# Kernel tuning notes

Measured on AMD Instinct MI355X. Metric: run time of the kernel, lower is better.

## Reference

```python
import jax, jax.numpy as jnp
import numpy as np

# Production-scale graph dims (see shape_source)
N = 50000      # nodes
E = 800000     # edges (avg degree 16)
C_IN = 128     # input feature dim
H = 96         # hidden (per species: prey X and predator Y)
C_OUT = 40     # num_classes
L = 5          # LVConv layers
DT = 0.05      # integration step


def setup_inputs() -> dict:
    key = jax.random.key(0)
    ks = jax.random.split(key, 14)
    x = jax.random.normal(ks[0], (N, C_IN), jnp.float32)
    edge_index = jax.random.randint(ks[1], (2, E), 0, N, dtype=jnp.int32)
    # lift linears
    Wx = jax.random.normal(ks[2], (C_IN, H), jnp.float32) / np.sqrt(C_IN)
    bx = jnp.zeros((H,), jnp.float32)
    Wy = jax.random.normal(ks[3], (C_IN, H), jnp.float32) / np.sqrt(C_IN)
    by = jnp.zeros((H,), jnp.float32)
    # per-layer Lotka-Volterra coefficients (per-channel), small positive scale
    alpha = 0.1 * jax.random.uniform(ks[4], (L, H), jnp.float32)
    beta  = 0.1 * jax.random.uniform(ks[5], (L, H), jnp.float32)
    gamma = 0.1 * jax.random.uniform(ks[6], (L, H), jnp.float32)
    delta = 0.1 * jax.random.uniform(ks[7], (L, H), jnp.float32)
    # readout on concat([X, Y])
    Wr = jax.random.normal(ks[8], (2 * H, C_OUT), jnp.float32) / np.sqrt(2 * H)
    br = jnp.zeros((C_OUT,), jnp.float32)
    return {"x": x, "edge_index": edge_index, "Wx": Wx, "bx": bx,
            "Wy": Wy, "by": by, "alpha": alpha, "beta": beta,
            "gamma": gamma, "delta": delta, "Wr": Wr, "br": br}


def reference(x, edge_index, Wx, bx, Wy, by, alpha, beta, gamma, delta, Wr, br):
    src, dst = edge_index[0], edge_index[1]
    # in-degree for mean aggregation over incoming edges
    deg = jax.ops.segment_sum(jnp.ones((E,), x.dtype), dst, num_segments=N)
    deg_inv = (1.0 / jnp.maximum(deg, 1.0))[:, None]  # [N,1]

    def mean_agg(v):  # [N,H] -> [N,H] neighbor mean (src -> dst)
        return jax.ops.segment_sum(v[src], dst, num_segments=N) * deg_inv

    # lift to prey (X) and predator (Y) populations
    X = jnp.tanh(x @ Wx + bx)
    Y = jnp.tanh(x @ Wy + by)
    # dropout is identity in eval mode (training=False)
    for l in range(L):
        aggX = mean_agg(X)
        aggY = mean_agg(Y)
        # explicit-Euler Lotka-Volterra dynamics on the graph
        Xn = X + DT * X * (alpha[l] - beta[l] * aggY)
        Yn = Y + DT * Y * (-gamma[l] + delta[l] * aggX)
        X, Y = Xn, Yn
    h = jnp.concatenate([X, Y], axis=-1)  # [N, 2H]
    return h @ Wr + br
```

## Files before the change

### kernel.cpp

```cpp
#include <hip/hip_runtime.h>
#include <hip/hip_bf16.h>
#include <hip/hip_fp16.h>


#define HDIM 96
#define CIN 128
#define COUT 40
#define NLAYER 5
#define DTC 0.05f

#define BK_SHIFT 7
#define BK_SIZE 128
#define EPB 4096

typedef float  vfloat2 __attribute__((ext_vector_type(2)));
typedef float  vfloat4 __attribute__((ext_vector_type(4)));
typedef short  vshort8 __attribute__((ext_vector_type(8)));

__device__ __forceinline__ unsigned bf16_rne(float f) {
    unsigned u = __float_as_uint(f);
    return (u + 0x7fffu + ((u >> 16) & 1u)) >> 16;
}

__device__ __forceinline__ unsigned pack_bf16_pair(float xf, float yf) {
    return bf16_rne(xf) | (bf16_rne(yf) << 16);
}

__device__ __forceinline__ unsigned pack_f16_pair(float a, float b) {
    unsigned ha = (unsigned)__half_as_ushort(__float2half_rn(a));
    unsigned hb = (unsigned)__half_as_ushort(__float2half_rn(b));
    return ha | (hb << 16);
}

__device__ __forceinline__ float f16_lo(unsigned u) {
    return __half2float(__ushort_as_half((unsigned short)(u & 0xffffu)));
}
__device__ __forceinline__ float f16_hi(unsigned u) {
    return __half2float(__ushort_as_half((unsigned short)(u >> 16)));
}

__device__ __forceinline__ unsigned pack_fp8_quad(float x0, float y0, float x1, float y1) {
    int lo = __builtin_amdgcn_cvt_pk_fp8_f32(x0, y0, 0, false);
    int full = __builtin_amdgcn_cvt_pk_fp8_f32(x1, y1, lo, true);
    return (unsigned)full;
}


__global__ __launch_bounds__(256) void bhist_kernel(const int* __restrict__ dst,
                                                    int* __restrict__ ghist, int E, int NB) {
    __shared__ int h[512];
    for (int i = threadIdx.x; i < NB; i += 256) h[i] = 0;
    __syncthreads();
    int base = blockIdx.x * EPB;
    int end = min(E, base + EPB);
    for (int e = base + threadIdx.x; e < end; e += 256)
        atomicAdd(&h[dst[e] >> BK_SHIFT], 1);
    __syncthreads();
    for (int i = threadIdx.x; i < NB; i += 256)
        if (h[i]) atomicAdd(&ghist[i], h[i]);
}

__global__ void bscan_kernel(const int* __restrict__ ghist, int* __restrict__ bbase,
                             int* __restrict__ bcursor, int* __restrict__ rowptr,
                             int NB, int N, int E) {
    __shared__ int sd[512];
    int t = threadIdx.x;
    int v = (t < NB) ? ghist[t] : 0;
    sd[t] = v;
    __syncthreads();
    for (int off = 1; off < 512; off <<= 1) {
        int tv = (t >= off) ? sd[t - off] : 0;
        __syncthreads();
        sd[t] += tv;
        __syncthreads();
    }
    if (t < NB) {
        int b = sd[t] - v;
        bbase[t] = b;
        bcursor[t] = b;
    }
    if (t == 0) { bbase[NB] = E; rowptr[N] = E; }
}

__global__ __launch_bounds__(256) void bscatter_kernel(
    const int* __restrict__ src, const int* __restrict__ dst,
    int* __restrict__ bcursor, unsigned* __restrict__ packed, int E, int NB) {
    __shared__ int h[512];
    __shared__ int cur[512];
    for (int i = threadIdx.x; i < NB; i += 256) h[i] = 0;
    __syncthreads();
    int base = blockIdx.x * EPB;
    int end = min(E, base + EPB);
    for (int e = base + threadIdx.x; e < end; e += 256)
        atomicAdd(&h[dst[e] >> BK_SHIFT], 1);
    __syncthreads();
    for (int i = threadIdx.x; i < NB; i += 256)
        cur[i] = h[i] ? atomicAdd(&bcursor[i], h[i]) : 0;
    __syncthreads();
    for (int e = base + threadIdx.x; e < end; e += 256) {
        int d = dst[e];
        int b = d >> BK_SHIFT;
        int pos = atomicAdd(&cur[b], 1);
        packed[pos] = (unsigned)src[e] | ((unsigned)(d & (BK_SIZE - 1)) << 17);
    }
}

__global__ __launch_bounds__(256) void bcsr_kernel(
    const unsigned* __restrict__ packed, const int* __restrict__ bbase,
    int* __restrict__ rowptr, float* __restrict__ dinv, int* __restrict__ csr,
    int N, int NB) {
    __shared__ int ldeg[BK_SIZE];
    __shared__ int sscan[BK_SIZE];
    __shared__ int lcur[BK_SIZE];
    int b = blockIdx.x;
    int t = threadIdx.x;
    int lo = bbase[b], hi = bbase[b + 1];
    if (t < BK_SIZE) ldeg[t] = 0;
    __syncthreads();
    for (int e = lo + t; e < hi; e += 256)
        atomicAdd(&ldeg[(packed[e] >> 17) & (BK_SIZE - 1)], 1);
    __syncthreads();
    if (t < BK_SIZE) sscan[t] = ldeg[t];
    __syncthreads();
    for (int off = 1; off < BK_SIZE; off <<= 1) {
        int tv = (t < BK_SIZE && t >= off) ? sscan[t - off] : 0;
        __syncthreads();
        if (t < BK_SIZE) sscan[t] += tv;
        __syncthreads();
    }
    if (t < BK_SIZE) {
        int excl = sscan[t] - ldeg[t];
        int gpos = lo + excl;
        lcur[t] = gpos;
        int node = b * BK_SIZE + t;
        if (node < N) {
            rowptr[node] = gpos;
            dinv[node] = 1.0f / fmaxf((float)ldeg[t], 1.0f);
        }
    }
    __syncthreads();
    for (int e = lo + t; e < hi; e += 256) {
        unsigned p = packed[e];
        int l = (p >> 17) & (BK_SIZE - 1);
        int pos = atomicAdd(&lcur[l], 1);
        csr[pos] = (int)(p & 0x1FFFFu);
    }
}


__global__ __launch_bounds__(256) void wprep_kernel(
    const float* __restrict__ Wx, const float* __restrict__ bx,
    const float* __restrict__ Wy, const float* __restrict__ by,
    unsigned short* __restrict__ WcT, float* __restrict__ bc) {
    int t = blockIdx.x * blockDim.x + threadIdx.x;
    if (t < 192 * 128) {
        int cc = t >> 7;
        int k = t & 127;
        int h = cc >> 1;
        float w = (cc & 1) ? Wy[k * HDIM + h] : Wx[k * HDIM + h];
        WcT[cc * 128 + k] = (unsigned short)bf16_rne(w);
    }
    if (t < 192) {
        int h = t >> 1;
        bc[t] = (t & 1) ? by[h] : bx[h];
    }
}


#define LW_STRIDE 136

__global__ __launch_bounds__(256) void lift_mfma_kernel(
    const float* __restrict__ x, const unsigned short* __restrict__ WcT,
    const float* __restrict__ bc, unsigned* __restrict__ S,
    unsigned* __restrict__ F, int N) {
    __shared__ unsigned short sW[192 * LW_STRIDE];
    __shared__ float sBc[192];
    int t = threadIdx.x;

    {
        const unsigned* g = (const unsigned*)WcT;
        unsigned* s = (unsigned*)sW;
        for (int i = t; i < 192 * 64; i += 256) {
            int cc = i >> 6;
            int kp = i & 63;
            s[cc * (LW_STRIDE / 2) + kp] = g[i];
        }
    }
    if (t < 192) sBc[t] = bc[t];
    __syncthreads();

    int wv = t >> 6;
    int lane = t & 63;
    int quad = lane >> 4;
    int m = lane & 15;
    int mbase = blockIdx.x * 64 + wv * 16;

    int anode = mbase + m;
    if (anode >= N) anode = N - 1;
    const float* xrow = x + (size_t)anode * CIN;

    vfloat4 acc[12];
#pragma unroll
    for (int i = 0; i < 12; i++) acc[i] = (vfloat4){0.f, 0.f, 0.f, 0.f};

#pragma unroll
    for (int kt = 0; kt < 4; kt++) {
        int k0 = kt * 32 + quad * 8;
        float4 xa = *(const float4*)(xrow + k0);
        float4 xb = *(const float4*)(xrow + k0 + 4);
        uint4 ua;
        ua.x = pack_bf16_pair(xa.x, xa.y);
        ua.y = pack_bf16_pair(xa.z, xa.w);
        ua.z = pack_bf16_pair(xb.x, xb.y);
        ua.w = pack_bf16_pair(xb.z, xb.w);
        vshort8 a = *(vshort8*)&ua;
#pragma unroll
        for (int nt = 0; nt < 12; nt++) {
            vshort8 b = *(const vshort8*)&sW[(nt * 16 + m) * LW_STRIDE + k0];
            acc[nt] = __builtin_amdgcn_mfma_f32_16x16x32_bf16(a, b, acc[nt], 0, 0, 0);
        }
    }

#pragma unroll
    for (int nt = 0; nt < 12; nt++) {
        int ccb = nt * 16 + m;
        float bco = sBc[ccb];
#pragma unroll
        for (int r = 0; r < 4; r++) {
            int node = mbase + quad * 4 + r;
            float v = tanhf(acc[nt][r] + bco);
            float v1 = __shfl_xor(v, 1);
            unsigned u = (unsigned)(__builtin_amdgcn_cvt_pk_fp8_f32(v, v1, 0, false) & 0xffff);
            unsigned w = u | (((unsigned)__shfl_xor((int)u, 2)) << 16);
            unsigned hp = pack_f16_pair(v, v1);
            if (node < N) {
                if ((m & 1) == 0) S[(size_t)node * 96 + (ccb >> 1)] = hp;
                if ((m & 3) == 0) F[(size_t)node * 48 + (ccb >> 2)] = w;
            }
        }
    }
}


#define LWPB 4

__global__ __launch_bounds__(256) void layer_kernel(
    const unsigned* __restrict__ F, const unsigned* __restrict__ S,
    unsigned* __restrict__ Sn, unsigned* __restrict__ Fn,
    const int* __restrict__ rowptr, const int* __restrict__ csr,
    const float* __restrict__ deg_inv,
    const float* __restrict__ alpha, const float* __restrict__ beta,
    const float* __restrict__ gamma, const float* __restrict__ delta,
    int N) {
    int wave = threadIdx.x >> 6;
    int lane = threadIdx.x & 63;
    int node = blockIdx.x * LWPB + wave;
    if (node >= N) return;

    int beg = rowptr[node];
    int cnt = rowptr[node + 1] - beg;
    bool act = (lane < 48);

    float ax0 = 0.f, ay0 = 0.f, ax1 = 0.f, ay1 = 0.f;

#define UNPACK_ACC(u)                                                      \
    do {                                                                   \
        vfloat2 p0 = __builtin_amdgcn_cvt_pk_f32_fp8((int)(u), false);     \
        vfloat2 p1 = __builtin_amdgcn_cvt_pk_f32_fp8((int)(u), true);      \
        ax0 += p0.x; ay0 += p0.y; ax1 += p1.x; ay1 += p1.y;                \
    } while (0)

    for (int base = 0; base < cnt; base += 64) {
        int m = min(64, cnt - base);
        int sidx = (lane < m) ? csr[beg + base + lane] : 0;
        int j = 0;
        for (; j + 8 <= m; j += 8) {
            int s0 = __shfl(sidx, j);
            int s1 = __shfl(sidx, j + 1);
            int s2 = __shfl(sidx, j + 2);
            int s3 = __shfl(sidx, j + 3);
            int s4 = __shfl(sidx, j + 4);
            int s5 = __shfl(sidx, j + 5);
            int s6 = __shfl(sidx, j + 6);
            int s7 = __shfl(sidx, j + 7);
            if (act) {
                unsigned u0 = F[(size_t)s0 * 48 + lane];
                unsigned u1 = F[(size_t)s1 * 48 + lane];
                unsigned u2 = F[(size_t)s2 * 48 + lane];
                unsigned u3 = F[(size_t)s3 * 48 + lane];
                unsigned u4 = F[(size_t)s4 * 48 + lane];
                unsigned u5 = F[(size_t)s5 * 48 + lane];
                unsigned u6 = F[(size_t)s6 * 48 + lane];
                unsigned u7 = F[(size_t)s7 * 48 + lane];
                UNPACK_ACC(u0); UNPACK_ACC(u1); UNPACK_ACC(u2); UNPACK_ACC(u3);
                UNPACK_ACC(u4); UNPACK_ACC(u5); UNPACK_ACC(u6); UNPACK_ACC(u7);
            }
        }
        for (; j < m; j++) {
            int s = __shfl(sidx, j);
            if (act) {
                unsigned u = F[(size_t)s * 48 + lane];
                UNPACK_ACC(u);
            }
        }
    }
#undef UNPACK_ACC

    float dinv = deg_inv[node];
    if (act) {
        ax0 *= dinv; ay0 *= dinv; ax1 *= dinv; ay1 *= dinv;
        float2 a2 = ((const float2*)alpha)[lane];
        float2 b2 = ((const float2*)beta)[lane];
        float2 g2 = ((const float2*)gamma)[lane];
        float2 d2 = ((const float2*)delta)[lane];
        uint2 su = ((const uint2*)(S + (size_t)node * 96))[lane];
        float vx = f16_lo(su.x), vy = f16_hi(su.x);
        float vz = f16_lo(su.y), vw = f16_hi(su.y);
        float ox = vx + DTC * vx * (a2.x - b2.x * ay0);
        float oy = vy + DTC * vy * (-g2.x + d2.x * ax0);
        float oz = vz + DTC * vz * (a2.y - b2.y * ay1);
        float ow = vw + DTC * vw * (-g2.y + d2.y * ax1);
        ((uint2*)(Sn + (size_t)node * 96))[lane] =
            make_uint2(pack_f16_pair(ox, oy), pack_f16_pair(oz, ow));
        if (Fn)
            Fn[(size_t)node * 48 + lane] = pack_fp8_quad(ox, oy, oz, ow);
    }
}


#define WG_STRIDE 200

__global__ __launch_bounds__(256) void readout_mfma_kernel(
    const unsigned short* __restrict__ sh, const float* __restrict__ Wr,
    const float* __restrict__ br, float* __restrict__ out, int N) {
    __shared__ unsigned short sW[48 * WG_STRIDE];
    __shared__ float sB[48];
    int t = threadIdx.x;

    for (int i = t; i < 48 * 192; i += 256) {
        int n = i / 192;
        int kk = i - n * 192;
        int h = kk >> 1;
        float w = 0.f;
        if (n < COUT) w = (kk & 1) ? Wr[(HDIM + h) * COUT + n] : Wr[h * COUT + n];
        sW[n * WG_STRIDE + kk] = __half_as_ushort(__float2half_rn(w));
    }
    if (t < 48) sB[t] = (t < COUT) ? br[t] : 0.f;
    __syncthreads();

    int wv = t >> 6;
    int lane = t & 63;
    int quad = lane >> 4;
    int m = lane & 15;
    int mbase = blockIdx.x * 64 + wv * 16;

    int anode = mbase + m;
    if (anode >= N) anode = N - 1;
    const unsigned short* arow = sh + (size_t)anode * 192;

    vfloat4 acc0 = {0.f, 0.f, 0.f, 0.f};
    vfloat4 acc1 = {0.f, 0.f, 0.f, 0.f};
    vfloat4 acc2 = {0.f, 0.f, 0.f, 0.f};

#pragma unroll
    for (int kt = 0; kt < 6; kt++) {
        int k0 = kt * 32 + quad * 8;
        vshort8 a = *(const vshort8*)(arow + k0);
        vshort8 b0 = *(const vshort8*)&sW[(0 * 16 + m) * WG_STRIDE + k0];
        vshort8 b1 = *(const vshort8*)&sW[(1 * 16 + m) * WG_STRIDE + k0];
        vshort8 b2 = *(const vshort8*)&sW[(2 * 16 + m) * WG_STRIDE + k0];
        acc0 = __builtin_amdgcn_mfma_f32_16x16x32_f16(a, b0, acc0, 0, 0, 0);
        acc1 = __builtin_amdgcn_mfma_f32_16x16x32_f16(a, b1, acc1, 0, 0, 0);
        acc2 = __builtin_amdgcn_mfma_f32_16x16x32_f16(a, b2, acc2, 0, 0, 0);
    }

    float bo0 = sB[m];
    float bo1 = sB[16 + m];
    float bo2 = (m < 8) ? sB[32 + m] : 0.f;
#pragma unroll
    for (int r = 0; r < 4; r++) {
        int node = mbase + quad * 4 + r;
        if (node < N) {
            float* orow = out + (size_t)node * COUT;
            orow[m] = acc0[r] + bo0;
            orow[16 + m] = acc1[r] + bo1;
            if (m < 8) orow[32 + m] = acc2[r] + bo2;
        }
    }
}


extern "C" void kernel_launch(void* const* d_in, const int* in_sizes, int n_in,
                              void* d_out, int out_size, void* d_ws, size_t ws_size,
                              hipStream_t stream) {
    const float* x     = (const float*)d_in[0];
    const int*   ei    = (const int*)d_in[1];
    const float* Wx    = (const float*)d_in[2];
    const float* bx    = (const float*)d_in[3];
    const float* Wy    = (const float*)d_in[4];
    const float* by    = (const float*)d_in[5];
    const float* alpha = (const float*)d_in[6];
    const float* beta  = (const float*)d_in[7];
    const float* gamma = (const float*)d_in[8];
    const float* delta = (const float*)d_in[9];
    const float* Wr    = (const float*)d_in[10];
    const float* br    = (const float*)d_in[11];

    const int N = in_sizes[0] / CIN;
    const int E = in_sizes[1] / 2;
    const int NB = (N + BK_SIZE - 1) >> BK_SHIFT;
    const int nchunk = (E + EPB - 1) / EPB;

    char* ws = (char*)d_ws;
    size_t off = 0;
    auto alloc = [&](size_t bytes) -> void* {
        off = (off + 255) & ~(size_t)255;
        void* p = ws + off;
        off += bytes;
        return p;
    };
    int* ghist     = (int*)alloc((size_t)NB * sizeof(int));
    int* bbase     = (int*)alloc((size_t)(NB + 1) * sizeof(int));
    int* bcursor   = (int*)alloc((size_t)NB * sizeof(int));
    unsigned* pckd = (unsigned*)alloc((size_t)E * sizeof(unsigned));
    int* rowptr    = (int*)alloc((size_t)(N + 1) * sizeof(int));
    int* csr       = (int*)alloc((size_t)E * sizeof(int));
    float* dinv    = (float*)alloc((size_t)N * sizeof(float));
    unsigned* Sa   = (unsigned*)alloc((size_t)N * 96 * sizeof(unsigned));
    unsigned* Sb   = (unsigned*)alloc((size_t)N * 96 * sizeof(unsigned));
    unsigned* Fa   = (unsigned*)alloc((size_t)N * 48 * sizeof(unsigned));
    unsigned* Fb   = (unsigned*)alloc((size_t)N * 48 * sizeof(unsigned));
    unsigned short* WcT = (unsigned short*)alloc((size_t)192 * 128 * sizeof(unsigned short));
    float* bc      = (float*)alloc((size_t)192 * sizeof(float));
    (void)ws_size;

    const int* e_src = ei;
    const int* e_dst = ei + E;

    hipMemsetAsync(ghist, 0, (size_t)NB * sizeof(int), stream);

    bhist_kernel<<<nchunk, 256, 0, stream>>>(e_dst, ghist, E, NB);
    bscan_kernel<<<1, 512, 0, stream>>>(ghist, bbase, bcursor, rowptr, NB, N, E);
    bscatter_kernel<<<nchunk, 256, 0, stream>>>(e_src, e_dst, bcursor, pckd, E, NB);
    bcsr_kernel<<<NB, 256, 0, stream>>>(pckd, bbase, rowptr, dinv, csr, N, NB);

    wprep_kernel<<<(192 * 128 + 255) / 256, 256, 0, stream>>>(Wx, bx, Wy, by, WcT, bc);
    lift_mfma_kernel<<<(N + 63) / 64, 256, 0, stream>>>(x, WcT, bc, Sa, Fa, N);

    const unsigned* Sc = Sa;
    unsigned* Snx = Sb;
    const unsigned* Fc = Fa;
    unsigned* Fnx = Fb;
    for (int l = 0; l < NLAYER; l++) {
        bool last = (l == NLAYER - 1);
        layer_kernel<<<(N + LWPB - 1) / LWPB, LWPB * 64, 0, stream>>>(
            Fc, Sc, Snx, last ? (unsigned*)nullptr : Fnx,
            rowptr, csr, dinv,
            alpha + l * HDIM, beta + l * HDIM, gamma + l * HDIM, delta + l * HDIM, N);
        const unsigned* ts = Sc; Sc = Snx; Snx = (unsigned*)ts;
        const unsigned* tf = Fc; Fc = Fnx; Fnx = (unsigned*)tf;
    }

    readout_mfma_kernel<<<(N + 63) / 64, 256, 0, stream>>>(
        (const unsigned short*)Sc, Wr, br, (float*)d_out, N);
}
```

Baseline: 354.7 us.

## Process four nodes per wave with 16-lane groups and 12-byte gathers

The layer kernel now assigns one 16-lane group per node, so each wave handles four nodes instead of one. Each lane fetches three packed fp8 words (uint3) per neighbor row, where before 48 of 64 lanes fetched one word each. This removes idle lanes and cuts per-node wave overhead, and it issues more independent loads per wave. In exchange, each lane holds more accumulator registers, neighbor loops inside a wave diverge when degrees differ, and the 12-byte accesses may be less aligned.

```diff
diff --git a/kernel.cpp b/kernel.cpp
--- a/kernel.cpp
+++ b/kernel.cpp
@@ -242,8 +242,6 @@
 }
 
 
-#define LWPB 4
-
 __global__ __launch_bounds__(256) void layer_kernel(
     const unsigned* __restrict__ F, const unsigned* __restrict__ S,
     unsigned* __restrict__ Sn, unsigned* __restrict__ Fn,
@@ -254,76 +252,85 @@
     int N) {
     int wave = threadIdx.x >> 6;
     int lane = threadIdx.x & 63;
-    int node = blockIdx.x * LWPB + wave;
-    if (node >= N) return;
-
-    int beg = rowptr[node];
-    int cnt = rowptr[node + 1] - beg;
-    bool act = (lane < 48);
-
-    float ax0 = 0.f, ay0 = 0.f, ax1 = 0.f, ay1 = 0.f;
-
-#define UNPACK_ACC(u)                                                      \
-    do {                                                                   \
-        vfloat2 p0 = __builtin_amdgcn_cvt_pk_f32_fp8((int)(u), false);     \
-        vfloat2 p1 = __builtin_amdgcn_cvt_pk_f32_fp8((int)(u), true);      \
-        ax0 += p0.x; ay0 += p0.y; ax1 += p1.x; ay1 += p1.y;                \
+    int li = lane & 15;
+    int gbase = lane & 48;
+
+    int node = (blockIdx.x * 4 + wave) * 4 + (lane >> 4);
+    bool nvalid = node < N;
+    int nclamp = nvalid ? node : N - 1;
+    int beg = rowptr[nclamp];
+    int cnt = nvalid ? (rowptr[nclamp + 1] - beg) : 0;
+
+    float ac[12];
+#pragma unroll
+    for (int i = 0; i < 12; i++) ac[i] = 0.f;
+
+#define UNP(u, k)                                                           \
+    do {                                                                    \
+        vfloat2 p0 = __builtin_amdgcn_cvt_pk_f32_fp8((int)(u), false);      \
+        vfloat2 p1 = __builtin_amdgcn_cvt_pk_f32_fp8((int)(u), true);       \
+        ac[4*(k)+0] += p0.x; ac[4*(k)+1] += p0.y;                           \
+        ac[4*(k)+2] += p1.x; ac[4*(k)+3] += p1.y;                           \
     } while (0)
-
-    for (int base = 0; base < cnt; base += 64) {
-        int m = min(64, cnt - base);
-        int sidx = (lane < m) ? csr[beg + base + lane] : 0;
+#define UNP3(u)  do { UNP((u).x, 0); UNP((u).y, 1); UNP((u).z, 2); } while (0)
+
+    for (int base = 0; base < cnt; base += 16) {
+        int m = min(16, cnt - base);
+        int sidx = (li < m) ? csr[beg + base + li] : 0;
         int j = 0;
-        for (; j + 8 <= m; j += 8) {
-            int s0 = __shfl(sidx, j);
-            int s1 = __shfl(sidx, j + 1);
-            int s2 = __shfl(sidx, j + 2);
-            int s3 = __shfl(sidx, j + 3);
-            int s4 = __shfl(sidx, j + 4);
-            int s5 = __shfl(sidx, j + 5);
-            int s6 = __shfl(sidx, j + 6);
-            int s7 = __shfl(sidx, j + 7);
-            if (act) {
-                unsigned u0 = F[(size_t)s0 * 48 + lane];
-                unsigned u1 = F[(size_t)s1 * 48 + lane];
-                unsigned u2 = F[(size_t)s2 * 48 + lane];
-                unsigned u3 = F[(size_t)s3 * 48 + lane];
-                unsigned u4 = F[(size_t)s4 * 48 + lane];
-                unsigned u5 = F[(size_t)s5 * 48 + lane];
-                unsigned u6 = F[(size_t)s6 * 48 + lane];
-                unsigned u7 = F[(size_t)s7 * 48 + lane];
-                UNPACK_ACC(u0); UNPACK_ACC(u1); UNPACK_ACC(u2); UNPACK_ACC(u3);
-                UNPACK_ACC(u4); UNPACK_ACC(u5); UNPACK_ACC(u6); UNPACK_ACC(u7);
-            }
+        for (; j + 4 <= m; j += 4) {
+            int s0 = __shfl(sidx, gbase + j);
+            int s1 = __shfl(sidx, gbase + j + 1);
+            int s2 = __shfl(sidx, gbase + j + 2);
+            int s3 = __shfl(sidx, gbase + j + 3);
+            uint3 u0 = ((const uint3*)(F + (size_t)s0 * 48))[li];
+            uint3 u1 = ((const uint3*)(F + (size_t)s1 * 48))[li];
+            uint3 u2 = ((const uint3*)(F + (size_t)s2 * 48))[li];
+            uint3 u3 = ((const uint3*)(F + (size_t)s3 * 48))[li];
+            UNP3(u0); UNP3(u1); UNP3(u2); UNP3(u3);
         }
         for (; j < m; j++) {
-            int s = __shfl(sidx, j);
-            if (act) {
-                unsigned u = F[(size_t)s * 48 + lane];
-                UNPACK_ACC(u);
-            }
-        }
-    }
-#undef UNPACK_ACC
-
-    float dinv = deg_inv[node];
-    if (act) {
-        ax0 *= dinv; ay0 *= dinv; ax1 *= dinv; ay1 *= dinv;
-        float2 a2 = ((const float2*)alpha)[lane];
-        float2 b2 = ((const float2*)beta)[lane];
-        float2 g2 = ((const float2*)gamma)[lane];
-        float2 d2 = ((const float2*)delta)[lane];
-        uint2 su = ((const uint2*)(S + (size_t)node * 96))[lane];
+            int s = __shfl(sidx, gbase + j);
+            uint3 u = ((const uint3*)(F + (size_t)s * 48))[li];
+            UNP3(u);
+        }
+    }
+#undef UNP3
+#undef UNP
+
+    if (!nvalid) return;
+
+    float dinv = deg_inv[nclamp];
+    const uint2* srow = (const uint2*)(S + (size_t)node * 96);
+    unsigned so[6];
+    unsigned fo[3];
+#pragma unroll
+    for (int k = 0; k < 3; k++) {
+        int p = 3 * li + k;
+        float2 a2 = ((const float2*)alpha)[p];
+        float2 b2 = ((const float2*)beta)[p];
+        float2 g2 = ((const float2*)gamma)[p];
+        float2 d2 = ((const float2*)delta)[p];
+        uint2 su = srow[p];
         float vx = f16_lo(su.x), vy = f16_hi(su.x);
         float vz = f16_lo(su.y), vw = f16_hi(su.y);
-        float ox = vx + DTC * vx * (a2.x - b2.x * ay0);
-        float oy = vy + DTC * vy * (-g2.x + d2.x * ax0);
-        float oz = vz + DTC * vz * (a2.y - b2.y * ay1);
-        float ow = vw + DTC * vw * (-g2.y + d2.y * ax1);
-        ((uint2*)(Sn + (size_t)node * 96))[lane] =
-            make_uint2(pack_f16_pair(ox, oy), pack_f16_pair(oz, ow));
-        if (Fn)
-            Fn[(size_t)node * 48 + lane] = pack_fp8_quad(ox, oy, oz, ow);
+        float ox = vx + DTC * vx * (a2.x - b2.x * (ac[4*k+1] * dinv));
+        float oy = vy + DTC * vy * (-g2.x + d2.x * (ac[4*k+0] * dinv));
+        float oz = vz + DTC * vz * (a2.y - b2.y * (ac[4*k+3] * dinv));
+        float ow = vw + DTC * vw * (-g2.y + d2.y * (ac[4*k+2] * dinv));
+        so[2*k+0] = pack_f16_pair(ox, oy);
+        so[2*k+1] = pack_f16_pair(oz, ow);
+        fo[k] = pack_fp8_quad(ox, oy, oz, ow);
+    }
+    {
+        uint3 t0 = {so[0], so[1], so[2]};
+        uint3 t1 = {so[3], so[4], so[5]};
+        ((uint3*)(Sn + (size_t)node * 96))[2*li+0] = t0;
+        ((uint3*)(Sn + (size_t)node * 96))[2*li+1] = t1;
+    }
+    if (Fn) {
+        uint3 tf = {fo[0], fo[1], fo[2]};
+        ((uint3*)(Fn + (size_t)node * 48))[li] = tf;
     }
 }
 
@@ -453,7 +460,7 @@
     unsigned* Fnx = Fb;
     for (int l = 0; l < NLAYER; l++) {
         bool last = (l == NLAYER - 1);
-        layer_kernel<<<(N + LWPB - 1) / LWPB, LWPB * 64, 0, stream>>>(
+        layer_kernel<<<(N + 15) / 16, 256, 0, stream>>>(
             Fc, Sc, Snx, last ? (unsigned*)nullptr : Fnx,
             rowptr, csr, dinv,
             alpha + l * HDIM, beta + l * HDIM, gamma + l * HDIM, delta + l * HDIM, N);
```

New measurement: 323.9 us. 8.7% less time.
